# Kernel tuning notes

Measured on AMD Instinct MI355X. Metric: run time of the kernel, lower is better.

Reference implementation:

```python
import jax, jax.numpy as jnp
import numpy as np

N = 40000      # nodes
E = 640000     # edges
IN_DIM = 128
HID = 128
HEADS = 4
DHEAD = HID // HEADS  # 32
LAYERS = 3
TIMESTEPS = 2
NEG_SLOPE = 0.2


def setup_inputs() -> dict:
    key = jax.random.key(0)
    ks = jax.random.split(key, 16)
    s = 0.05
    inp = {
        "node_feats": jax.random.normal(ks[0], (N, IN_DIM), jnp.float32),
        "src": jax.random.randint(ks[1], (E,), 0, N, jnp.int32),
        "dst": jax.random.randint(ks[2], (E,), 0, N, jnp.int32),
        "proj_W": jax.random.normal(ks[3], (IN_DIM, HID), jnp.float32) * s,
        "proj_b": jnp.zeros((HID,), jnp.float32),
        "fc_W": jax.random.normal(ks[4], (LAYERS, HID, HID), jnp.float32) * s,
        "attn_l": jax.random.normal(ks[5], (LAYERS, HEADS, DHEAD), jnp.float32) * s,
        "attn_r": jax.random.normal(ks[6], (LAYERS, HEADS, DHEAD), jnp.float32) * s,
        "conv_bias": jnp.zeros((LAYERS, HID), jnp.float32),
        "gru_Wih": jax.random.normal(ks[7], (3 * HID, HID), jnp.float32) * s,
        "gru_Whh": jax.random.normal(ks[8], (3 * HID, HID), jnp.float32) * s,
        "gru_bih": jnp.zeros((3 * HID,), jnp.float32),
        "gru_bhh": jnp.zeros((3 * HID,), jnp.float32),
    }
    return inp


def _gat_layer(h, src, dst, fc_W, attn_l, attn_r, bias):
    # h: (N, HID). DGL GATConv: fc -> edge attn -> segment softmax -> scatter sum
    feat = (h @ fc_W).reshape(N, HEADS, DHEAD)
    el = jnp.einsum('nhd,hd->nh', feat, attn_l)  # (N, H)
    er = jnp.einsum('nhd,hd->nh', feat, attn_r)
    e = jax.nn.leaky_relu(el[src] + er[dst], NEG_SLOPE)  # (E, H)
    # segment softmax over incoming edges per destination node
    emax = jax.ops.segment_max(e, dst, num_segments=N)  # (N, H)
    ee = jnp.exp(e - emax[dst])
    denom = jax.ops.segment_sum(ee, dst, num_segments=N)
    alpha = ee / denom[dst]  # (E, H)
    msg = feat[src] * alpha[:, :, None]  # (E, H, D)
    rst = jax.ops.segment_sum(msg, dst, num_segments=N)  # (N, H, D)
    rst = rst + h.reshape(N, HEADS, DHEAD)          # identity residual
    rst = rst + bias.reshape(HEADS, DHEAD)          # learned bias
    return jax.nn.elu(rst).reshape(N, HID)


def _gru_step(x, Wih, Whh, bih, bhh):
    # seq_len == 1, h0 == 0 -> recurrent matmul Whh @ h0 vanishes; b_hh remains
    gi = x @ Wih.T + bih  # (N, 3*HID)
    r = jax.nn.sigmoid(gi[:, :HID] + bhh[:HID])
    z = jax.nn.sigmoid(gi[:, HID:2 * HID] + bhh[HID:2 * HID])
    n = jnp.tanh(gi[:, 2 * HID:] + r * bhh[2 * HID:])
    return (1.0 - z) * n


def reference(node_feats, src, dst, proj_W, proj_b, fc_W, attn_l, attn_r,
              conv_bias, gru_Wih, gru_Whh, gru_bih, gru_bhh):
    h = node_feats @ proj_W + proj_b
    for l in range(LAYERS):
        h = _gat_layer(h, src, dst, fc_W[l], attn_l[l], attn_r[l], conv_bias[l])
    for _ in range(TIMESTEPS):
        h = _gru_step(h, gru_Wih, gru_Whh, gru_bih, gru_bhh)
    return h
```

## Files before the change

### kernel.cpp

```cpp
#include <hip/hip_runtime.h>
#include <hip/hip_bf16.h>

#define NNODES 40000
#define NEDGES 640000
#define M2PAD  40064
#define HID    128
#define PADCAP 920064
#define WSTRIDE_P (PADCAP + 16)

typedef __attribute__((ext_vector_type(8))) short bf16x8;
typedef __attribute__((ext_vector_type(4))) float f32x4;

__device__ __forceinline__ float bl(unsigned u){ return __uint_as_float(u << 16); }
__device__ __forceinline__ float bh(unsigned u){ return __uint_as_float(u & 0xFFFF0000u); }
__device__ __forceinline__ unsigned short f2b(float f){
    unsigned u = __float_as_uint(f);
    u = (u + 0x7FFFu + ((u >> 16) & 1u)) >> 16;
    return (unsigned short)u;
}
__device__ __forceinline__ float fast_rcp(float x){ return __builtin_amdgcn_rcpf(x); }

__device__ __forceinline__ void g2l16(const void* g, void* l){
    __builtin_amdgcn_global_load_lds(
        (const __attribute__((address_space(1))) unsigned int*)g,
        (__attribute__((address_space(3))) unsigned int*)l, 16, 0, 0);
}

__global__ void prep_all(const float* __restrict__ node_feats,
                         const float* __restrict__ proj_W, const float* __restrict__ fc_W,
                         const float* __restrict__ gru_Wih, const int* __restrict__ dstp,
                         unsigned short* __restrict__ nf,
                         unsigned short* __restrict__ projWT, unsigned short* __restrict__ fcWT,
                         unsigned short* __restrict__ gruWb, int* __restrict__ deg){
    int b = blockIdx.x;
    if (b < 5000){
        int gid = b * 256 + threadIdx.x;
        float4 v = ((const float4*)node_feats)[gid];
        ushort4 o;
        o.x = f2b(v.x); o.y = f2b(v.y); o.z = f2b(v.z); o.w = f2b(v.w);
        ((ushort4*)nf)[gid] = o;
    } else if (b < 5256){
        int t = b - 5000;
        int c = t >> 6;
        int idx = (t & 63) * 256 + threadIdx.x;
        const float* in   = (c == 0) ? proj_W : fc_W + (size_t)(c - 1) * 16384;
        unsigned short* o = (c == 0) ? projWT : fcWT + (size_t)(c - 1) * 16384;
        int k = idx >> 7, n = idx & 127;
        o[n * 128 + k] = f2b(in[idx]);
    } else if (b < 5448){
        int idx = (b - 5256) * 256 + threadIdx.x;
        gruWb[idx] = f2b(gru_Wih[idx]);
    } else {
        int e = (b - 5448) * 256 + threadIdx.x;
        atomicAdd(&deg[dstp[e]], 1);
    }
}

__global__ __launch_bounds__(1024) void scan_kernel(const int* __restrict__ deg,
        int* __restrict__ rowptr, int* __restrict__ cur, int Nn4){
    __shared__ int wsum[17];
    __shared__ int carry;
    int t = threadIdx.x, lane = t & 63, wid = t >> 6;
    if (t == 0) carry = 0;
    __syncthreads();
    for (int base = 0; base < Nn4; base += 1024){
        int i4 = base + t;
        int4 dg = (i4 < Nn4) ? ((const int4*)deg)[i4] : make_int4(0, 0, 0, 0);
        int p0 = (dg.x + 7) & ~7, p1 = (dg.y + 7) & ~7;
        int p2 = (dg.z + 7) & ~7, p3 = (dg.w + 7) & ~7;
        int v = p0 + p1 + p2 + p3;
        int x = v;
        #pragma unroll
        for (int d = 1; d < 64; d <<= 1){
            int y = __shfl_up(x, d, 64);
            if (lane >= d) x += y;
        }
        if (lane == 63) wsum[wid] = x;
        __syncthreads();
        if (wid == 0){
            int vv = (lane < 16) ? wsum[lane] : 0;
            int xx = vv;
            #pragma unroll
            for (int d = 1; d < 16; d <<= 1){
                int y = __shfl_up(xx, d, 64);
                if (lane >= d) xx += y;
            }
            if (lane < 16) wsum[lane] = xx - vv;
            if (lane == 15) wsum[16] = xx;
        }
        __syncthreads();
        int excl = carry + wsum[wid] + (x - v);
        if (i4 < Nn4){
            int4 o = make_int4(excl, excl + p0, excl + p0 + p1, excl + p0 + p1 + p2);
            ((int4*)rowptr)[i4] = o;
            ((int4*)cur)[i4]    = o;
        }
        __syncthreads();
        if (t == 0) carry += wsum[16];
        __syncthreads();
    }
    if (t == 0) rowptr[Nn4 * 4] = carry;
}

__global__ void fill_kernel(const int* __restrict__ src, const int* __restrict__ dst,
                            int* __restrict__ cur, int* __restrict__ esrc,
                            int* __restrict__ edst){
    int e = blockIdx.x * 256 + threadIdx.x;
    int d = dst[e];
    int pos = atomicAdd(&cur[d], 1);
    esrc[pos] = src[e];
    edst[pos] = d;
}

template<int MT>
__global__ __launch_bounds__(256) void gemm_t(
        const unsigned short* __restrict__ A, const unsigned short* __restrict__ BT,
        const float* __restrict__ bias, void* __restrict__ C,
        int Mreal, int ldc, int outF32,
        const float* __restrict__ al, const float* __restrict__ ar,
        float* __restrict__ elp, float* __restrict__ erp)
{
    __shared__ unsigned char lds[MT * 256 + 32768];
    unsigned char* ldsA = lds;
    unsigned char* ldsB = lds + MT * 256;
    int w = threadIdx.x >> 6, lane = threadIdx.x & 63;
    int rsub = lane >> 4, c16 = lane & 15;
    long baseM = (long)blockIdx.x * MT;
    long baseN = (long)blockIdx.y * 128;

    #pragma unroll
    for (int i = 0; i < MT / 16; i++){
        int chunk = w * (MT / 16) + i;
        int r = chunk * 4 + rsub;
        int cg = c16 ^ (r & 15);
        long ar_ = baseM + r; if (ar_ >= Mreal) ar_ = Mreal - 1;
        g2l16((const unsigned char*)A + ar_ * 256 + cg * 16, ldsA + chunk * 1024);
    }
    #pragma unroll
    for (int i = 0; i < 8; i++){
        int chunk = w * 8 + i;
        int r = chunk * 4 + rsub;
        int cg = c16 ^ (r & 15);
        long br = baseN + r;
        g2l16((const unsigned char*)BT + br * 256 + cg * 16, ldsB + chunk * 1024);
    }
    __syncthreads();

    constexpr int MI = 4;
    constexpr int NI = (MT == 128) ? 4 : 2;
    int mo = (MT == 128) ? (w & 1) * 64 : 0;
    int no = (MT == 128) ? (w >> 1) * 64 : w * 32;
    int q = lane >> 4, cl = lane & 15;
    f32x4 acc[MI][NI];
    #pragma unroll
    for (int i = 0; i < MI; i++)
        #pragma unroll
        for (int j = 0; j < NI; j++) acc[i][j] = (f32x4){0.f, 0.f, 0.f, 0.f};

    #pragma unroll
    for (int kc = 0; kc < 4; kc++){
        bf16x8 av[MI], bv[NI];
        #pragma unroll
        for (int mi = 0; mi < MI; mi++){
            int row = mo + mi * 16 + cl;
            int cs = (kc * 4 + q) ^ (row & 15);
            av[mi] = *(const bf16x8*)(ldsA + row * 256 + cs * 16);
        }
        #pragma unroll
        for (int ni = 0; ni < NI; ni++){
            int row = no + ni * 16 + cl;
            int cs = (kc * 4 + q) ^ (row & 15);
            bv[ni] = *(const bf16x8*)(ldsB + row * 256 + cs * 16);
        }
        #pragma unroll
        for (int mi = 0; mi < MI; mi++)
            #pragma unroll
            for (int ni = 0; ni < NI; ni++)
                acc[mi][ni] = __builtin_amdgcn_mfma_f32_16x16x32_bf16(av[mi], bv[ni], acc[mi][ni], 0, 0, 0);
    }

    #pragma unroll
    for (int mi = 0; mi < MI; mi++){
        #pragma unroll
        for (int ni = 0; ni < NI; ni++){
            int gn = (int)baseN + no + ni * 16 + cl;
            float bvf = bias ? bias[gn] : 0.f;
            long gm0 = baseM + mo + mi * 16 + q * 4;
            #pragma unroll
            for (int reg = 0; reg < 4; reg++){
                float v = acc[mi][ni][reg] + bvf;
                long gm = gm0 + reg;
                if (gm < Mreal){
                    if (outF32) ((float*)C)[gm * ldc + gn] = v;
                    else ((unsigned short*)C)[gm * ldc + gn] = f2b(v);
                }
            }
        }
    }

    if (NI == 2 && al){
        float al_lo = al[no + cl], al_hi = al[no + 16 + cl];
        float ar_lo = ar[no + cl], ar_hi = ar[no + 16 + cl];
        #pragma unroll
        for (int mi = 0; mi < MI; mi++){
            #pragma unroll
            for (int reg = 0; reg < 4; reg++){
                float pl = acc[mi][0][reg] * al_lo + acc[mi][1][reg] * al_hi;
                float pr = acc[mi][0][reg] * ar_lo + acc[mi][1][reg] * ar_hi;
                #pragma unroll
                for (int msk = 8; msk; msk >>= 1){
                    pl += __shfl_xor(pl, msk, 64);
                    pr += __shfl_xor(pr, msk, 64);
                }
                long gm = baseM + mi * 16 + q * 4 + reg;
                if (cl == 0 && gm < Mreal){
                    elp[gm * 4 + w] = pl;
                    erp[gm * 4 + w] = pr;
                }
            }
        }
    }
}

__global__ __launch_bounds__(256) void gru_fused(
        const unsigned short* __restrict__ A, const unsigned short* __restrict__ BT,
        const float* __restrict__ bih, const float* __restrict__ bhh,
        void* __restrict__ out, int Mreal, int outF32)
{
    __shared__ unsigned char ldsA[16384];
    __shared__ unsigned char ldsB[32768];
    int w = threadIdx.x >> 6, lane = threadIdx.x & 63;
    int rsub = lane >> 4, c16 = lane & 15;
    long baseM = (long)blockIdx.x * 64;

    #pragma unroll
    for (int i = 0; i < 4; i++){
        int chunk = w * 4 + i;
        int r = chunk * 4 + rsub;
        int cg = c16 ^ (r & 15);
        long ar = baseM + r; if (ar >= Mreal) ar = Mreal - 1;
        g2l16((const unsigned char*)A + ar * 256 + cg * 16, ldsA + chunk * 1024);
    }

    int no = w * 32;
    int q = lane >> 4, cl = lane & 15;
    f32x4 acc[3][4][2];
    #pragma unroll
    for (int c = 0; c < 3; c++)
        #pragma unroll
        for (int i = 0; i < 4; i++)
            #pragma unroll
            for (int j = 0; j < 2; j++) acc[c][i][j] = (f32x4){0.f, 0.f, 0.f, 0.f};

    for (int c = 0; c < 3; c++){
        if (c) __syncthreads();
        #pragma unroll
        for (int i = 0; i < 8; i++){
            int chunk = w * 8 + i;
            int r = chunk * 4 + rsub;
            int cg = c16 ^ (r & 15);
            long br = c * 128 + r;
            g2l16((const unsigned char*)BT + br * 256 + cg * 16, ldsB + chunk * 1024);
        }
        __syncthreads();
        #pragma unroll
        for (int kc = 0; kc < 4; kc++){
            bf16x8 av[4], bv[2];
            #pragma unroll
            for (int mi = 0; mi < 4; mi++){
                int row = mi * 16 + cl;
                int cs = (kc * 4 + q) ^ (row & 15);
                av[mi] = *(const bf16x8*)(ldsA + row * 256 + cs * 16);
            }
            #pragma unroll
            for (int ni = 0; ni < 2; ni++){
                int row = no + ni * 16 + cl;
                int cs = (kc * 4 + q) ^ (row & 15);
                bv[ni] = *(const bf16x8*)(ldsB + row * 256 + cs * 16);
            }
            #pragma unroll
            for (int mi = 0; mi < 4; mi++)
                #pragma unroll
                for (int ni = 0; ni < 2; ni++)
                    acc[c][mi][ni] = __builtin_amdgcn_mfma_f32_16x16x32_bf16(av[mi], bv[ni], acc[c][mi][ni], 0, 0, 0);
        }
    }

    #pragma unroll
    for (int ni = 0; ni < 2; ni++){
        int j = no + ni * 16 + cl;
        float bir = bih[j]       + bhh[j];
        float biz = bih[128 + j] + bhh[128 + j];
        float bin = bih[256 + j];
        float bhn = bhh[256 + j];
        #pragma unroll
        for (int mi = 0; mi < 4; mi++){
            long gm0 = baseM + mi * 16 + q * 4;
            #pragma unroll
            for (int reg = 0; reg < 4; reg++){
                long n_row = gm0 + reg;
                float gr = acc[0][mi][ni][reg] + bir;
                float gz = acc[1][mi][ni][reg] + biz;
                float gn = acc[2][mi][ni][reg] + bin;
                float r = fast_rcp(1.f + __expf(-gr));
                float z = fast_rcp(1.f + __expf(-gz));
                float ex = __expf(2.f * (gn + r * bhn));
                float nn = (ex - 1.f) * fast_rcp(ex + 1.f);
                float v = (1.f - z) * nn;
                if (n_row < Mreal){
                    if (outF32) ((float*)out)[n_row * 128 + j] = v;
                    else ((unsigned short*)out)[n_row * 128 + j] = f2b(v);
                }
            }
        }
    }
}

__global__ void edge_w(const int* __restrict__ esrc, const int* __restrict__ edst,
                       const float* __restrict__ el, const float* __restrict__ er,
                       float* __restrict__ wgtT){
    int p = blockIdx.x * 256 + threadIdx.x;
    int dn = edst[p];
    if (dn < 0){
        wgtT[0 * WSTRIDE_P + p] = 0.f;
        wgtT[1 * WSTRIDE_P + p] = 0.f;
        wgtT[2 * WSTRIDE_P + p] = 0.f;
        wgtT[3 * WSTRIDE_P + p] = 0.f;
        return;
    }
    int sn = esrc[p];
    float4 l = *(const float4*)(el + (size_t)sn * 4);
    float4 r = *(const float4*)(er + (size_t)dn * 4);
    float e;
    e = l.x + r.x; e = (e > 0.f) ? e : 0.2f * e; wgtT[0 * WSTRIDE_P + p] = __expf(e);
    e = l.y + r.y; e = (e > 0.f) ? e : 0.2f * e; wgtT[1 * WSTRIDE_P + p] = __expf(e);
    e = l.z + r.z; e = (e > 0.f) ? e : 0.2f * e; wgtT[2 * WSTRIDE_P + p] = __expf(e);
    e = l.w + r.w; e = (e > 0.f) ? e : 0.2f * e; wgtT[3 * WSTRIDE_P + p] = __expf(e);
}

__global__ __launch_bounds__(256) void aggregate(
        const int* __restrict__ rowptr, const int* __restrict__ esrc,
        const float* __restrict__ wgtT,
        const unsigned short* __restrict__ feat, const float* __restrict__ bias,
        unsigned short* __restrict__ h)
{
    int wid = threadIdx.x >> 6, lane = threadIdx.x & 63;
    int n = blockIdx.x * 4 + wid;
    int hh = lane >> 4;
    int d0 = lane * 2;
    unsigned doff = (unsigned)(d0 * 2);
    int beg = rowptr[n], end = rowptr[n + 1];
    float s = 0.f, a0 = 0.f, a1 = 0.f;
    const char* fbc = (const char*)feat;
    const float* wp = wgtT + (size_t)hh * WSTRIDE_P + beg;
    const int*   ep = esrc + beg;

    if (beg < end){
        int4 sA = *(const int4*)(ep);
        int4 sB = *(const int4*)(ep + 4);
        float4 wA = make_float4(0.f,0.f,0.f,0.f), wB = wA;
        unsigned f0=0,f1=0,f2=0,f3=0,f4=0,f5=0,f6=0,f7=0;
        for (int p = beg; p < end; p += 8){
            float4 wcA = *(const float4*)(wp);
            float4 wcB = *(const float4*)(wp + 4);
            unsigned c0 = *(const unsigned*)(fbc + ((((unsigned)sA.x) << 8) + doff));
            unsigned c1 = *(const unsigned*)(fbc + ((((unsigned)sA.y) << 8) + doff));
            unsigned c2 = *(const unsigned*)(fbc + ((((unsigned)sA.z) << 8) + doff));
            unsigned c3 = *(const unsigned*)(fbc + ((((unsigned)sA.w) << 8) + doff));
            unsigned c4 = *(const unsigned*)(fbc + ((((unsigned)sB.x) << 8) + doff));
            unsigned c5 = *(const unsigned*)(fbc + ((((unsigned)sB.y) << 8) + doff));
            unsigned c6 = *(const unsigned*)(fbc + ((((unsigned)sB.z) << 8) + doff));
            unsigned c7 = *(const unsigned*)(fbc + ((((unsigned)sB.w) << 8) + doff));
            int4 nA = *(const int4*)(ep + 8);
            int4 nB = *(const int4*)(ep + 12);
            s += ((wA.x + wA.y) + (wA.z + wA.w)) + ((wB.x + wB.y) + (wB.z + wB.w));
            a0 = fmaf(wA.x, bl(f0), fmaf(wA.y, bl(f1), fmaf(wA.z, bl(f2), fmaf(wA.w, bl(f3), a0))));
            a0 = fmaf(wB.x, bl(f4), fmaf(wB.y, bl(f5), fmaf(wB.z, bl(f6), fmaf(wB.w, bl(f7), a0))));
            a1 = fmaf(wA.x, bh(f0), fmaf(wA.y, bh(f1), fmaf(wA.z, bh(f2), fmaf(wA.w, bh(f3), a1))));
            a1 = fmaf(wB.x, bh(f4), fmaf(wB.y, bh(f5), fmaf(wB.z, bh(f6), fmaf(wB.w, bh(f7), a1))));
            wA = wcA; wB = wcB;
            f0 = c0; f1 = c1; f2 = c2; f3 = c3; f4 = c4; f5 = c5; f6 = c6; f7 = c7;
            sA = nA; sB = nB;
            wp += 8; ep += 8;
        }
        s += ((wA.x + wA.y) + (wA.z + wA.w)) + ((wB.x + wB.y) + (wB.z + wB.w));
        a0 = fmaf(wA.x, bl(f0), fmaf(wA.y, bl(f1), fmaf(wA.z, bl(f2), fmaf(wA.w, bl(f3), a0))));
        a0 = fmaf(wB.x, bl(f4), fmaf(wB.y, bl(f5), fmaf(wB.z, bl(f6), fmaf(wB.w, bl(f7), a0))));
        a1 = fmaf(wA.x, bh(f0), fmaf(wA.y, bh(f1), fmaf(wA.z, bh(f2), fmaf(wA.w, bh(f3), a1))));
        a1 = fmaf(wB.x, bh(f4), fmaf(wB.y, bh(f5), fmaf(wB.z, bh(f6), fmaf(wB.w, bh(f7), a1))));
    }
    float inv = (s > 0.f) ? fast_rcp(s) : 0.f;
    unsigned hv = *(const unsigned*)(h + (size_t)n * 128 + d0);
    float x0 = a0 * inv + bl(hv) + bias[d0];
    float x1 = a1 * inv + bh(hv) + bias[d0 + 1];
    x0 = (x0 > 0.f) ? x0 : expm1f(x0);
    x1 = (x1 > 0.f) ? x1 : expm1f(x1);
    unsigned outv = (unsigned)f2b(x0) | ((unsigned)f2b(x1) << 16);
    *(unsigned*)(h + (size_t)n * 128 + d0) = outv;
}

extern "C" void kernel_launch(void* const* d_in, const int* in_sizes, int n_in,
                              void* d_out, int out_size, void* d_ws, size_t ws_size,
                              hipStream_t stream) {
    const float* node_feats = (const float*)d_in[0];
    const int*   srcp       = (const int*)d_in[1];
    const int*   dstp       = (const int*)d_in[2];
    const float* proj_W     = (const float*)d_in[3];
    const float* proj_b     = (const float*)d_in[4];
    const float* fc_W       = (const float*)d_in[5];
    const float* attn_l     = (const float*)d_in[6];
    const float* attn_r     = (const float*)d_in[7];
    const float* conv_bias  = (const float*)d_in[8];
    const float* gru_Wih    = (const float*)d_in[9];
    const float* gru_bih    = (const float*)d_in[11];
    const float* gru_bhh    = (const float*)d_in[12];
    float* outp = (float*)d_out;

    char* ws = (char*)d_ws;
    size_t off = 0;
    auto carve = [&](size_t bytes) -> char* {
        char* p = ws + off;
        off += (bytes + 255) & ~(size_t)255;
        return p;
    };
    int*            deg    = (int*)carve((size_t)NNODES * 4);
    int*            rowptr = (int*)carve((size_t)(NNODES + 1) * 4);
    int*            cur    = (int*)carve((size_t)NNODES * 4);
    int*            esrc   = (int*)carve((size_t)(PADCAP + 32) * 4);
    int*            edst   = (int*)carve((size_t)PADCAP * 4);
    float*          el     = (float*)carve((size_t)NNODES * 4 * 4);
    float*          er     = (float*)carve((size_t)NNODES * 4 * 4);
    float*          wgtT   = (float*)carve((size_t)4 * WSTRIDE_P * 4);
    unsigned short* projWT = (unsigned short*)carve(16384 * 2);
    unsigned short* fcWT   = (unsigned short*)carve(3 * 16384 * 2);
    unsigned short* gruWb  = (unsigned short*)carve(49152 * 2);
    unsigned short* nf     = (unsigned short*)carve((size_t)NNODES * 128 * 2);
    unsigned short* h      = (unsigned short*)carve((size_t)M2PAD * 128 * 2);
    unsigned short* feat   = (unsigned short*)carve((size_t)M2PAD * 128 * 2);
    (void)ws_size; (void)in_sizes; (void)n_in; (void)out_size;

    hipMemsetAsync(deg, 0, (size_t)NNODES * 4, stream);
    hipMemsetAsync(esrc, 0, (size_t)(PADCAP + 32) * 4, stream);
    hipMemsetAsync(edst, 0xFF, (size_t)PADCAP * 4, stream);
    prep_all<<<7948, 256, 0, stream>>>(node_feats, proj_W, fc_W, gru_Wih, dstp,
                                       nf, projWT, fcWT, gruWb, deg);
    scan_kernel<<<1, 1024, 0, stream>>>(deg, rowptr, cur, NNODES / 4);
    fill_kernel<<<NEDGES / 256, 256, 0, stream>>>(srcp, dstp, cur, esrc, edst);

    gemm_t<64><<<dim3(625, 1), 256, 0, stream>>>(nf, projWT, proj_b, h, NNODES, 128, 0,
                                                 nullptr, nullptr, nullptr, nullptr);

    for (int l = 0; l < 3; l++){
        gemm_t<64><<<dim3(625, 1), 256, 0, stream>>>(h, fcWT + l * 16384, nullptr, feat, NNODES, 128, 0,
                                                     attn_l + l * 128, attn_r + l * 128, el, er);
        edge_w<<<PADCAP / 256, 256, 0, stream>>>(esrc, edst, el, er, wgtT);
        aggregate<<<NNODES / 4, 256, 0, stream>>>(rowptr, esrc, wgtT, feat, conv_bias + l * 128, h);
    }

    gru_fused<<<625, 256, 0, stream>>>(h, gruWb, gru_bih, gru_bhh, h, NNODES, 0);
    gru_fused<<<625, 256, 0, stream>>>(h, gruWb, gru_bih, gru_bhh, outp, NNODES, 1);
}
```

Before: 369.3 us.

## Fuse edge attention weight computation into aggregation kernel

Removes the separate edge_w kernel and the wgtT buffer. Each aggregation now gathers el of the source node and er of the destination node and computes the leaky-relu and exp inline, masking padded slots by degree. The edst array and its memset go away. This saves three kernel launches and the write and reread of the per-edge weight array. In exchange it adds scattered el gathers and exp work inside the aggregation loop, which is repeated per lane.

```diff
diff --git a/kernel.cpp b/kernel.cpp
--- a/kernel.cpp
+++ b/kernel.cpp
@@ -6,7 +6,6 @@
 #define M2PAD  40064
 #define HID    128
 #define PADCAP 920064
-#define WSTRIDE_P (PADCAP + 16)
 
 typedef __attribute__((ext_vector_type(8))) short bf16x8;
 typedef __attribute__((ext_vector_type(4))) float f32x4;
@@ -24,6 +23,13 @@
     __builtin_amdgcn_global_load_lds(
         (const __attribute__((address_space(1))) unsigned int*)g,
         (__attribute__((address_space(3))) unsigned int*)l, 16, 0, 0);
+}
+
+__device__ __forceinline__ float wcalc(float e, float erw, int j, int rem){
+    float t = e + erw;
+    t = (t > 0.f) ? t : 0.2f * t;
+    t = __expf(t);
+    return (j < rem) ? t : 0.f;
 }
 
 __global__ void prep_all(const float* __restrict__ node_feats,
@@ -103,13 +109,11 @@
 }
 
 __global__ void fill_kernel(const int* __restrict__ src, const int* __restrict__ dst,
-                            int* __restrict__ cur, int* __restrict__ esrc,
-                            int* __restrict__ edst){
+                            int* __restrict__ cur, int* __restrict__ esrc){
     int e = blockIdx.x * 256 + threadIdx.x;
     int d = dst[e];
     int pos = atomicAdd(&cur[d], 1);
     esrc[pos] = src[e];
-    edst[pos] = d;
 }
 
 template<int MT>
@@ -316,31 +320,10 @@
     }
 }
 
-__global__ void edge_w(const int* __restrict__ esrc, const int* __restrict__ edst,
-                       const float* __restrict__ el, const float* __restrict__ er,
-                       float* __restrict__ wgtT){
-    int p = blockIdx.x * 256 + threadIdx.x;
-    int dn = edst[p];
-    if (dn < 0){
-        wgtT[0 * WSTRIDE_P + p] = 0.f;
-        wgtT[1 * WSTRIDE_P + p] = 0.f;
-        wgtT[2 * WSTRIDE_P + p] = 0.f;
-        wgtT[3 * WSTRIDE_P + p] = 0.f;
-        return;
-    }
-    int sn = esrc[p];
-    float4 l = *(const float4*)(el + (size_t)sn * 4);
-    float4 r = *(const float4*)(er + (size_t)dn * 4);
-    float e;
-    e = l.x + r.x; e = (e > 0.f) ? e : 0.2f * e; wgtT[0 * WSTRIDE_P + p] = __expf(e);
-    e = l.y + r.y; e = (e > 0.f) ? e : 0.2f * e; wgtT[1 * WSTRIDE_P + p] = __expf(e);
-    e = l.z + r.z; e = (e > 0.f) ? e : 0.2f * e; wgtT[2 * WSTRIDE_P + p] = __expf(e);
-    e = l.w + r.w; e = (e > 0.f) ? e : 0.2f * e; wgtT[3 * WSTRIDE_P + p] = __expf(e);
-}
-
 __global__ __launch_bounds__(256) void aggregate(
-        const int* __restrict__ rowptr, const int* __restrict__ esrc,
-        const float* __restrict__ wgtT,
+        const int* __restrict__ rowptr, const int* __restrict__ degv,
+        const int* __restrict__ esrc,
+        const float* __restrict__ el, const float* __restrict__ er,
         const unsigned short* __restrict__ feat, const float* __restrict__ bias,
         unsigned short* __restrict__ h)
 {
@@ -350,19 +333,28 @@
     int d0 = lane * 2;
     unsigned doff = (unsigned)(d0 * 2);
     int beg = rowptr[n], end = rowptr[n + 1];
+    int dg  = degv[n];
+    float erw = er[(size_t)n * 4 + hh];
     float s = 0.f, a0 = 0.f, a1 = 0.f;
     const char* fbc = (const char*)feat;
-    const float* wp = wgtT + (size_t)hh * WSTRIDE_P + beg;
-    const int*   ep = esrc + beg;
+    const int*  ep  = esrc + beg;
 
     if (beg < end){
         int4 sA = *(const int4*)(ep);
         int4 sB = *(const int4*)(ep + 4);
-        float4 wA = make_float4(0.f,0.f,0.f,0.f), wB = wA;
+        float e0=0.f,e1=0.f,e2=0.f,e3=0.f,e4=0.f,e5=0.f,e6=0.f,e7=0.f;
         unsigned f0=0,f1=0,f2=0,f3=0,f4=0,f5=0,f6=0,f7=0;
+        int rprev = 0;
+        int rcur  = dg;
         for (int p = beg; p < end; p += 8){
-            float4 wcA = *(const float4*)(wp);
-            float4 wcB = *(const float4*)(wp + 4);
+            float g0 = el[(((unsigned)sA.x) << 2) + hh];
+            float g1 = el[(((unsigned)sA.y) << 2) + hh];
+            float g2 = el[(((unsigned)sA.z) << 2) + hh];
+            float g3 = el[(((unsigned)sA.w) << 2) + hh];
+            float g4 = el[(((unsigned)sB.x) << 2) + hh];
+            float g5 = el[(((unsigned)sB.y) << 2) + hh];
+            float g6 = el[(((unsigned)sB.z) << 2) + hh];
+            float g7 = el[(((unsigned)sB.w) << 2) + hh];
             unsigned c0 = *(const unsigned*)(fbc + ((((unsigned)sA.x) << 8) + doff));
             unsigned c1 = *(const unsigned*)(fbc + ((((unsigned)sA.y) << 8) + doff));
             unsigned c2 = *(const unsigned*)(fbc + ((((unsigned)sA.z) << 8) + doff));
@@ -373,21 +365,38 @@
             unsigned c7 = *(const unsigned*)(fbc + ((((unsigned)sB.w) << 8) + doff));
             int4 nA = *(const int4*)(ep + 8);
             int4 nB = *(const int4*)(ep + 12);
-            s += ((wA.x + wA.y) + (wA.z + wA.w)) + ((wB.x + wB.y) + (wB.z + wB.w));
-            a0 = fmaf(wA.x, bl(f0), fmaf(wA.y, bl(f1), fmaf(wA.z, bl(f2), fmaf(wA.w, bl(f3), a0))));
-            a0 = fmaf(wB.x, bl(f4), fmaf(wB.y, bl(f5), fmaf(wB.z, bl(f6), fmaf(wB.w, bl(f7), a0))));
-            a1 = fmaf(wA.x, bh(f0), fmaf(wA.y, bh(f1), fmaf(wA.z, bh(f2), fmaf(wA.w, bh(f3), a1))));
-            a1 = fmaf(wB.x, bh(f4), fmaf(wB.y, bh(f5), fmaf(wB.z, bh(f6), fmaf(wB.w, bh(f7), a1))));
-            wA = wcA; wB = wcB;
+            float w0 = wcalc(e0, erw, 0, rprev);
+            float w1 = wcalc(e1, erw, 1, rprev);
+            float w2 = wcalc(e2, erw, 2, rprev);
+            float w3 = wcalc(e3, erw, 3, rprev);
+            float w4 = wcalc(e4, erw, 4, rprev);
+            float w5 = wcalc(e5, erw, 5, rprev);
+            float w6 = wcalc(e6, erw, 6, rprev);
+            float w7 = wcalc(e7, erw, 7, rprev);
+            s += ((w0 + w1) + (w2 + w3)) + ((w4 + w5) + (w6 + w7));
+            a0 = fmaf(w0, bl(f0), fmaf(w1, bl(f1), fmaf(w2, bl(f2), fmaf(w3, bl(f3), a0))));
+            a0 = fmaf(w4, bl(f4), fmaf(w5, bl(f5), fmaf(w6, bl(f6), fmaf(w7, bl(f7), a0))));
+            a1 = fmaf(w0, bh(f0), fmaf(w1, bh(f1), fmaf(w2, bh(f2), fmaf(w3, bh(f3), a1))));
+            a1 = fmaf(w4, bh(f4), fmaf(w5, bh(f5), fmaf(w6, bh(f6), fmaf(w7, bh(f7), a1))));
+            e0 = g0; e1 = g1; e2 = g2; e3 = g3; e4 = g4; e5 = g5; e6 = g6; e7 = g7;
             f0 = c0; f1 = c1; f2 = c2; f3 = c3; f4 = c4; f5 = c5; f6 = c6; f7 = c7;
             sA = nA; sB = nB;
-            wp += 8; ep += 8;
-        }
-        s += ((wA.x + wA.y) + (wA.z + wA.w)) + ((wB.x + wB.y) + (wB.z + wB.w));
-        a0 = fmaf(wA.x, bl(f0), fmaf(wA.y, bl(f1), fmaf(wA.z, bl(f2), fmaf(wA.w, bl(f3), a0))));
-        a0 = fmaf(wB.x, bl(f4), fmaf(wB.y, bl(f5), fmaf(wB.z, bl(f6), fmaf(wB.w, bl(f7), a0))));
-        a1 = fmaf(wA.x, bh(f0), fmaf(wA.y, bh(f1), fmaf(wA.z, bh(f2), fmaf(wA.w, bh(f3), a1))));
-        a1 = fmaf(wB.x, bh(f4), fmaf(wB.y, bh(f5), fmaf(wB.z, bh(f6), fmaf(wB.w, bh(f7), a1))));
+            rprev = rcur; rcur -= 8;
+            ep += 8;
+        }
+        float w0 = wcalc(e0, erw, 0, rprev);
+        float w1 = wcalc(e1, erw, 1, rprev);
+        float w2 = wcalc(e2, erw, 2, rprev);
+        float w3 = wcalc(e3, erw, 3, rprev);
+        float w4 = wcalc(e4, erw, 4, rprev);
+        float w5 = wcalc(e5, erw, 5, rprev);
+        float w6 = wcalc(e6, erw, 6, rprev);
+        float w7 = wcalc(e7, erw, 7, rprev);
+        s += ((w0 + w1) + (w2 + w3)) + ((w4 + w5) + (w6 + w7));
+        a0 = fmaf(w0, bl(f0), fmaf(w1, bl(f1), fmaf(w2, bl(f2), fmaf(w3, bl(f3), a0))));
+        a0 = fmaf(w4, bl(f4), fmaf(w5, bl(f5), fmaf(w6, bl(f6), fmaf(w7, bl(f7), a0))));
+        a1 = fmaf(w0, bh(f0), fmaf(w1, bh(f1), fmaf(w2, bh(f2), fmaf(w3, bh(f3), a1))));
+        a1 = fmaf(w4, bh(f4), fmaf(w5, bh(f5), fmaf(w6, bh(f6), fmaf(w7, bh(f7), a1))));
     }
     float inv = (s > 0.f) ? fast_rcp(s) : 0.f;
     unsigned hv = *(const unsigned*)(h + (size_t)n * 128 + d0);
@@ -427,10 +436,8 @@
     int*            rowptr = (int*)carve((size_t)(NNODES + 1) * 4);
     int*            cur    = (int*)carve((size_t)NNODES * 4);
     int*            esrc   = (int*)carve((size_t)(PADCAP + 32) * 4);
-    int*            edst   = (int*)carve((size_t)PADCAP * 4);
     float*          el     = (float*)carve((size_t)NNODES * 4 * 4);
     float*          er     = (float*)carve((size_t)NNODES * 4 * 4);
-    float*          wgtT   = (float*)carve((size_t)4 * WSTRIDE_P * 4);
     unsigned short* projWT = (unsigned short*)carve(16384 * 2);
     unsigned short* fcWT   = (unsigned short*)carve(3 * 16384 * 2);
     unsigned short* gruWb  = (unsigned short*)carve(49152 * 2);
@@ -441,11 +448,10 @@
 
     hipMemsetAsync(deg, 0, (size_t)NNODES * 4, stream);
     hipMemsetAsync(esrc, 0, (size_t)(PADCAP + 32) * 4, stream);
-    hipMemsetAsync(edst, 0xFF, (size_t)PADCAP * 4, stream);
     prep_all<<<7948, 256, 0, stream>>>(node_feats, proj_W, fc_W, gru_Wih, dstp,
                                        nf, projWT, fcWT, gruWb, deg);
     scan_kernel<<<1, 1024, 0, stream>>>(deg, rowptr, cur, NNODES / 4);
-    fill_kernel<<<NEDGES / 256, 256, 0, stream>>>(srcp, dstp, cur, esrc, edst);
+    fill_kernel<<<NEDGES / 256, 256, 0, stream>>>(srcp, dstp, cur, esrc);
 
     gemm_t<64><<<dim3(625, 1), 256, 0, stream>>>(nf, projWT, proj_b, h, NNODES, 128, 0,
                                                  nullptr, nullptr, nullptr, nullptr);
@@ -453,8 +459,8 @@
     for (int l = 0; l < 3; l++){
         gemm_t<64><<<dim3(625, 1), 256, 0, stream>>>(h, fcWT + l * 16384, nullptr, feat, NNODES, 128, 0,
                                                      attn_l + l * 128, attn_r + l * 128, el, er);
-        edge_w<<<PADCAP / 256, 256, 0, stream>>>(esrc, edst, el, er, wgtT);
-        aggregate<<<NNODES / 4, 256, 0, stream>>>(rowptr, esrc, wgtT, feat, conv_bias + l * 128, h);
+        aggregate<<<NNODES / 4, 256, 0, stream>>>(rowptr, deg, esrc, el, er, feat,
+                                                  conv_bias + l * 128, h);
     }
 
     gru_fused<<<625, 256, 0, stream>>>(h, gruWb, gru_bih, gru_bhh, h, NNODES, 0);
```

Measured after the change: 367.4 us. Within noise of the previous version (-0.5%).
